# Optimization experiments

Measured on AMD Instinct MI355X. Metric: run time of the kernel, lower is better.

Reference implementation:

```python
import jax, jax.numpy as jnp
import numpy as np

EPS = 1e-5

def _silu(x):
    return x * jax.nn.sigmoid(x)

def _layernorm(x, g, b):
    mu = jnp.mean(x, axis=-1, keepdims=True)
    var = jnp.mean((x - mu) ** 2, axis=-1, keepdims=True)
    return (x - mu) * jax.lax.rsqrt(var + EPS) * g + b

def _mamba(x, in_w, conv_w, conv_b, xproj_w, dt_w, dt_b, A_log, Dp, out_w):
    # x: (B, L, dm); faithful mamba-ssm block: in_proj -> causal dwconv -> silu ->
    # x_proj -> softplus(dt_proj) -> selective scan -> gate -> out_proj
    B, L, dm = x.shape
    di, K = conv_w.shape          # d_inner, d_conv
    ds = A_log.shape[1]           # d_state
    dtr = dt_w.shape[1]           # dt_rank
    xz = x @ in_w.T               # (B, L, 2*di)
    xi, z = jnp.split(xz, 2, axis=-1)
    # causal depthwise conv1d (pad K-1 on the left), kernel unrolled (K=4)
    xpad = jnp.pad(xi, ((0, 0), (K - 1, 0), (0, 0)))
    xc = conv_b + sum(conv_w[:, k] * xpad[:, k:k + L, :] for k in range(K))
    xc = _silu(xc)                # (B, L, di)
    xdbl = xc @ xproj_w.T         # (B, L, dtr + 2*ds)
    dt, Bm, Cm = jnp.split(xdbl, [dtr, dtr + ds], axis=-1)
    delta = jax.nn.softplus(dt @ dt_w.T + dt_b)        # (B, L, di)
    A = -jnp.exp(A_log)                                # (di, ds)
    dA = jnp.exp(delta[..., None] * A)                 # (B, L, di, ds)
    dBu = delta[..., None] * Bm[:, :, None, :] * xc[..., None]
    def step(h, inp):
        dA_t, dBu_t, C_t = inp                         # (B,di,ds),(B,di,ds),(B,ds)
        h = dA_t * h + dBu_t
        y = jnp.einsum('bdn,bn->bd', h, C_t)
        return h, y
    h0 = jnp.zeros((B, di, ds), dtype=x.dtype)
    _, ys = jax.lax.scan(step, h0, (dA.transpose(1, 0, 2, 3),
                                    dBu.transpose(1, 0, 2, 3),
                                    Cm.transpose(1, 0, 2)))
    y = ys.transpose(1, 0, 2) + xc * Dp                # (B, L, di)
    y = y * _silu(z)
    return y @ out_w.T                                 # (B, L, dm)

def _forward(t1, t2, t3, t4, t5,
             m0_in_w, m0_conv_w, m0_conv_b, m0_xproj_w, m0_dt_w, m0_dt_b, m0_Alog, m0_D, m0_out_w,
             m1_in_w, m1_conv_w, m1_conv_b, m1_xproj_w, m1_dt_w, m1_dt_b, m1_Alog, m1_D, m1_out_w,
             norm_g, norm_b, proj_w, proj_b, norm1_g, norm1_b, proj1_w, proj1_b, skip_scale):
    B = t1.shape[0]
    flat = lambda t, c: t.reshape(B, c, -1).transpose(0, 2, 1)   # (B, N, C)
    f1, f2, f3, f4, f5 = flat(t1, 8), flat(t2, 16), flat(t3, 24), flat(t4, 32), flat(t5, 48)
    c1 = jnp.concatenate([f1[:, :, 0:8], f2[:, :, 0:8], f3[:, :, 0:8], f4[:, :, 0:8], f5[:, :, 0:8]], axis=1)   # (B,21824,8)
    c2 = jnp.concatenate([f2[:, :, 8:16], f3[:, :, 8:16], f4[:, :, 8:16], f5[:, :, 8:16]], axis=1)              # (B,5440,8)
    c3 = jnp.concatenate([f3[:, :, 16:24], f4[:, :, 16:24], f5[:, :, 16:24]], axis=1)                           # (B,1344,8)
    c4 = jnp.concatenate([f4[:, :, 24:32], f5[:, :, 24:32]], axis=1)                                            # (B,320,8)
    c5 = f5[:, :, 32:48]                                                                                        # (B,64,16)
    def block8(c):
        y = _mamba(c, m0_in_w, m0_conv_w, m0_conv_b, m0_xproj_w, m0_dt_w, m0_dt_b, m0_Alog, m0_D, m0_out_w)
        return _layernorm(y + skip_scale * c, norm_g, norm_b) @ proj_w.T + proj_b
    x1m, x2m, x3m, x4m = block8(c1), block8(c2), block8(c3), block8(c4)
    y5 = _mamba(c5, m1_in_w, m1_conv_w, m1_conv_b, m1_xproj_w, m1_dt_w, m1_dt_b, m1_Alog, m1_D, m1_out_w)
    x5m = _layernorm(y5 + skip_scale * c5, norm1_g, norm1_b) @ proj1_w.T + proj1_b
    a1 = x1m[:, 0:16384, :]
    a2 = jnp.concatenate([x1m[:, 16384:20480, :], x2m[:, 0:4096, :]], axis=2)
    a3 = jnp.concatenate([x1m[:, 20480:21504, :], x2m[:, 4096:5120, :], x3m[:, 0:1024, :]], axis=2)
    a4 = jnp.concatenate([x1m[:, 21504:21760, :], x2m[:, 5120:5376, :], x3m[:, 1024:1280, :], x4m[:, 0:256, :]], axis=2)
    a5 = jnp.concatenate([x1m[:, 21760:, :], x2m[:, 5376:, :], x3m[:, 1280:, :], x4m[:, 256:, :], x5m], axis=2)
    x1 = a1.transpose(0, 2, 1).reshape(B, 8, 128, 128)
    x2 = a2.transpose(0, 2, 1).reshape(B, 16, 64, 64)
    x3 = a3.transpose(0, 2, 1).reshape(B, 24, 32, 32)
    x4 = a4.transpose(0, 2, 1).reshape(B, 32, 16, 16)
    x5 = a5.transpose(0, 2, 1).reshape(B, 48, 8, 8)
    return (x1, x2, x3, x4, x5)

def setup_inputs() -> dict:
    key = jax.random.key(0)
    ks = iter(jax.random.split(key, 64))
    B = 8
    def n(shape, s=1.0):
        return jax.random.normal(next(ks), shape, dtype=jnp.float32) * s
    inp = {
        't1': n((B, 8, 128, 128)), 't2': n((B, 16, 64, 64)), 't3': n((B, 24, 32, 32)),
        't4': n((B, 32, 16, 16)), 't5': n((B, 48, 8, 8)),
    }
    def mamba_params(pfx, dm):
        di, ds, K, dtr = 2 * dm, 16, 4, 1  # expand=2, d_state=16, d_conv=4, dt_rank=ceil(dm/16)=1
        return {
            pfx + '_in_w': n((2 * di, dm), dm ** -0.5),
            pfx + '_conv_w': n((di, K), 0.3),
            pfx + '_conv_b': n((di,), 0.1),
            pfx + '_xproj_w': n((dtr + 2 * ds, di), di ** -0.5),
            pfx + '_dt_w': n((di, dtr), 1.0),
            pfx + '_dt_b': n((di,), 0.1) - 3.0,
            pfx + '_Alog': jnp.log(jnp.tile(jnp.arange(1.0, ds + 1.0, dtype=jnp.float32), (di, 1))),
            pfx + '_D': jnp.ones((di,), jnp.float32),
            pfx + '_out_w': n((dm, di), di ** -0.5),
        }
    inp.update(mamba_params('m0', 8))
    inp.update(mamba_params('m1', 16))
    inp.update({
        'norm_g': jnp.ones((8,), jnp.float32), 'norm_b': jnp.zeros((8,), jnp.float32),
        'proj_w': n((8, 8), 8 ** -0.5), 'proj_b': jnp.zeros((8,), jnp.float32),
        'norm1_g': jnp.ones((16,), jnp.float32), 'norm1_b': jnp.zeros((16,), jnp.float32),
        'proj1_w': n((16, 16), 16 ** -0.5), 'proj1_b': jnp.zeros((16,), jnp.float32),
        'skip_scale': jnp.ones((1,), jnp.float32),
    })
    return inp

def reference(t1, t2, t3, t4, t5,
              m0_in_w, m0_conv_w, m0_conv_b, m0_xproj_w, m0_dt_w, m0_dt_b, m0_Alog, m0_D, m0_out_w,
              m1_in_w, m1_conv_w, m1_conv_b, m1_xproj_w, m1_dt_w, m1_dt_b, m1_Alog, m1_D, m1_out_w,
              norm_g, norm_b, proj_w, proj_b, norm1_g, norm1_b, proj1_w, proj1_b, skip_scale):
    return _forward(t1, t2, t3, t4, t5,
                    m0_in_w, m0_conv_w, m0_conv_b, m0_xproj_w, m0_dt_w, m0_dt_b, m0_Alog, m0_D, m0_out_w,
                    m1_in_w, m1_conv_w, m1_conv_b, m1_xproj_w, m1_dt_w, m1_dt_b, m1_Alog, m1_D, m1_out_w,
                    norm_g, norm_b, proj_w, proj_b, norm1_g, norm1_b, proj1_w, proj1_b, skip_scale)
```

## Files before the change

kernel.cpp:

```cpp
#include <hip/hip_runtime.h>
#include <cmath>

#define SCH 128
#define SUB 32
#define NCB 228
#define NCHUNK 1824
#define NSUB 7296
#define CPB 2
#define NBLK 912
#define SW_IN 0
#define SW_CONVW 256
#define SW_CONVB 320
#define SW_XPROJ 336
#define SW_DTW 864
#define SW_DTB 880
#define SW_A 896
#define SW_D 1152
#define SW_OUTW 1168
#define SW_NG 1296
#define SW_NB 1304
#define SW_PW 1312
#define SW_PB 1376
#define SW_SKIP 1384
#define REC 1392
#define XP8 5872
#define GRECW 5004
#define YOF 6396
#define SMEM3 8572
#define V_IN 0
#define V_CONVW 1024
#define V_CONVB 1152
#define V_XPROJ 1184
#define V_DTW 2240
#define V_DTB 2272
#define V_A 2304
#define V_D 2816
#define V_OUTW 2848
#define V_NG 3360
#define V_NB 3376
#define V_PW 3392
#define V_PB 3648
#define V_SKIP 3664
#define V_XC 3668
#define V_DL 5780
#define V_BM 7892
#define V_CM 8916
#define SMEMP1 9940

struct Params {
  const float *t0, *t1, *t2, *t3, *t4;
  const float *in_w0,*conv_w0,*conv_b0,*xproj0,*dtw0,*dtb0,*Alog0,*D0,*outw0;
  const float *in_w1,*conv_w1,*conv_b1,*xproj1,*dtw1,*dtb1,*Alog1,*D1,*outw1;
  const float *ng,*nb,*pw,*pb,*n1g,*n1b,*p1w,*p1b,*skip;
  float* out;
  float *hloc, *sumdelta, *grec;
};

__device__ __forceinline__ float softplusf(float x) { return x > 20.f ? x : log1pf(__expf(x)); }
__device__ __forceinline__ float siluf(float x) { return x * (1.f / (1.f + __expf(-x))); }
__device__ __forceinline__ unsigned pk(float a, float b) {
  unsigned ua = __float_as_uint(a) + 0x8000u;
  unsigned ub = __float_as_uint(b) + 0x8000u;
  return (ua >> 16) | (ub & 0xFFFF0000u);
}
__device__ __forceinline__ float lo16(unsigned w) { return __uint_as_float(w << 16); }
__device__ __forceinline__ float hi16(unsigned w) { return __uint_as_float(w & 0xFFFF0000u); }

struct Loc { int k, pos, ch, hw, C; };

__device__ __forceinline__ Loc locate(int seq, int l) {
  Loc r;
  if (seq == 0) { r.ch = 0;
    if (l < 16384)      { r.k=0; r.pos=l;        r.hw=16384; r.C=8;  }
    else if (l < 20480) { r.k=1; r.pos=l-16384;  r.hw=4096;  r.C=16; }
    else if (l < 21504) { r.k=2; r.pos=l-20480;  r.hw=1024;  r.C=24; }
    else if (l < 21760) { r.k=3; r.pos=l-21504;  r.hw=256;   r.C=32; }
    else                { r.k=4; r.pos=l-21760;  r.hw=64;    r.C=48; }
  } else if (seq == 1) { r.ch = 8;
    if (l < 4096)       { r.k=1; r.pos=l;        r.hw=4096;  r.C=16; }
    else if (l < 5120)  { r.k=2; r.pos=l-4096;   r.hw=1024;  r.C=24; }
    else if (l < 5376)  { r.k=3; r.pos=l-5120;   r.hw=256;   r.C=32; }
    else                { r.k=4; r.pos=l-5376;   r.hw=64;    r.C=48; }
  } else if (seq == 2) { r.ch = 16;
    if (l < 1024)       { r.k=2; r.pos=l;        r.hw=1024;  r.C=24; }
    else if (l < 1280)  { r.k=3; r.pos=l-1024;   r.hw=256;   r.C=32; }
    else                { r.k=4; r.pos=l-1280;   r.hw=64;    r.C=48; }
  } else { r.ch = 24;
    if (l < 256)        { r.k=3; r.pos=l;        r.hw=256;   r.C=32; }
    else                { r.k=4; r.pos=l-256;    r.hw=64;    r.C=48; }
  }
  return r;
}

__device__ __forceinline__ const float* tsel(const Params& p, int k) {
  switch (k) { case 0: return p.t0; case 1: return p.t1; case 2: return p.t2;
               case 3: return p.t3; default: return p.t4; }
}
__device__ __forceinline__ int outbase(int k) {
  switch (k) { case 0: return 0; case 1: return 1048576; case 2: return 1572864;
               case 3: return 1769472; default: return 1835008; }
}

__device__ __forceinline__ void gather8(const Params& p, int b, int seq, int l, float* c) {
  Loc lc = locate(seq, l);
  const float* t = tsel(p, lc.k);
  int base = (b * lc.C + lc.ch) * lc.hw + lc.pos;
  #pragma unroll
  for (int j = 0; j < 8; ++j) c[j] = t[base + j * lc.hw];
}

__device__ __forceinline__ void decode_bid(int bid, int& b, int& seq, int& l0, int& Sa) {
  b = bid / NCB;
  int r = bid - b * NCB;
  int c, L;
  if (r < 171)      { seq = 0; c = r;       L = 21824; }
  else if (r < 214) { seq = 1; c = r - 171; L = 5440;  }
  else if (r < 225) { seq = 2; c = r - 214; L = 1344;  }
  else              { seq = 3; c = r - 225; L = 320;   }
  l0 = c * SCH;
  int rem = L - l0;
  Sa = rem < SCH ? rem : SCH;
}

__device__ void load_w0(const Params& p, float* s, int tid) {
  for (int i = tid; i < 256; i += 256) s[SW_IN + i] = p.in_w0[i];
  for (int i = tid; i < 64;  i += 256) s[SW_CONVW + i] = p.conv_w0[i];
  for (int i = tid; i < 16;  i += 256) s[SW_CONVB + i] = p.conv_b0[i];
  for (int i = tid; i < 528; i += 256) s[SW_XPROJ + i] = p.xproj0[i];
  for (int i = tid; i < 16;  i += 256) s[SW_DTW + i] = p.dtw0[i];
  for (int i = tid; i < 16;  i += 256) s[SW_DTB + i] = p.dtb0[i];
  for (int i = tid; i < 256; i += 256) s[SW_A + i] = -__expf(p.Alog0[i]);
  for (int i = tid; i < 16;  i += 256) s[SW_D + i] = p.D0[i];
  for (int i = tid; i < 128; i += 256) s[SW_OUTW + i] = p.outw0[i];
  for (int i = tid; i < 8;   i += 256) s[SW_NG + i] = p.ng[i];
  for (int i = tid; i < 8;   i += 256) s[SW_NB + i] = p.nb[i];
  for (int i = tid; i < 64;  i += 256) s[SW_PW + i] = p.pw[i];
  for (int i = tid; i < 8;   i += 256) s[SW_PB + i] = p.pb[i];
  if (tid == 0) s[SW_SKIP] = p.skip[0];
}

__device__ __forceinline__ float dot16h(const float* w, int ch0, int cho,
                                        const float* a, const float* o) {
  float4 wa0 = *(const float4*)&w[ch0];
  float4 wa1 = *(const float4*)&w[ch0 + 4];
  float4 wb0 = *(const float4*)&w[cho];
  float4 wb1 = *(const float4*)&w[cho + 4];
  float r = wa0.x * a[0];
  r = fmaf(wa0.y, a[1], r); r = fmaf(wa0.z, a[2], r); r = fmaf(wa0.w, a[3], r);
  r = fmaf(wa1.x, a[4], r); r = fmaf(wa1.y, a[5], r);
  r = fmaf(wa1.z, a[6], r); r = fmaf(wa1.w, a[7], r);
  r = fmaf(wb0.x, o[0], r); r = fmaf(wb0.y, o[1], r);
  r = fmaf(wb0.z, o[2], r); r = fmaf(wb0.w, o[3], r);
  r = fmaf(wb1.x, o[4], r); r = fmaf(wb1.y, o[5], r);
  r = fmaf(wb1.z, o[6], r); r = fmaf(wb1.w, o[7], r);
  return r;
}

__device__ void stage1(const Params& p, float* s, int b, int seq, int l0, int Sa, int tid) {
  int tok = tid >> 1, hf = tid & 1;
  int ch0 = hf * 8, cho = 8 - ch0;
  if (tok < Sa + 3) {
    int l = l0 - 3 + tok;
    float x8[8];
    if (l >= 0) gather8(p, b, seq, l, x8);
    else {
      #pragma unroll
      for (int j = 0; j < 8; ++j) x8[j] = 0.f;
    }
    #pragma unroll
    for (int ii = 0; ii < 8; ++ii) {
      int i = ch0 + ii;
      float4 wa = *(const float4*)&s[SW_IN + i * 8];
      float4 wb = *(const float4*)&s[SW_IN + i * 8 + 4];
      float a = wa.x * x8[0];
      a = fmaf(wa.y, x8[1], a); a = fmaf(wa.z, x8[2], a); a = fmaf(wa.w, x8[3], a);
      a = fmaf(wb.x, x8[4], a); a = fmaf(wb.y, x8[5], a);
      a = fmaf(wb.z, x8[6], a); a = fmaf(wb.w, x8[7], a);
      s[REC + tok * 17 + i] = a;
    }
    if (hf == 0) {
      unsigned* xp = (unsigned*)&s[XP8 + tok * 4];
      #pragma unroll
      for (int q = 0; q < 4; ++q) xp[q] = pk(x8[2*q], x8[2*q + 1]);
    }
  }
  if (Sa == SCH && tok >= SCH - 3) {
    int r = tok + 3;
    int l = l0 - 3 + r;
    float x8[8];
    gather8(p, b, seq, l, x8);
    #pragma unroll
    for (int ii = 0; ii < 8; ++ii) {
      int i = ch0 + ii;
      float4 wa = *(const float4*)&s[SW_IN + i * 8];
      float4 wb = *(const float4*)&s[SW_IN + i * 8 + 4];
      float a = wa.x * x8[0];
      a = fmaf(wa.y, x8[1], a); a = fmaf(wa.z, x8[2], a); a = fmaf(wa.w, x8[3], a);
      a = fmaf(wb.x, x8[4], a); a = fmaf(wb.y, x8[5], a);
      a = fmaf(wb.z, x8[6], a); a = fmaf(wb.w, x8[7], a);
      s[REC + r * 17 + i] = a;
    }
    if (hf == 0) {
      unsigned* xp = (unsigned*)&s[XP8 + r * 4];
      #pragma unroll
      for (int q = 0; q < 4; ++q) xp[q] = pk(x8[2*q], x8[2*q + 1]);
    }
  }
  __syncthreads();
  bool act = tok < Sa;
  float xc8[8], xco[8];
  float dt = 0.f;
  if (act) {
    #pragma unroll
    for (int ii = 0; ii < 8; ++ii) {
      int i = ch0 + ii;
      float4 cw = *(const float4*)&s[SW_CONVW + i * 4];
      float a = s[SW_CONVB + i];
      a = fmaf(cw.x, s[REC + (tok + 0) * 17 + i], a);
      a = fmaf(cw.y, s[REC + (tok + 1) * 17 + i], a);
      a = fmaf(cw.z, s[REC + (tok + 2) * 17 + i], a);
      a = fmaf(cw.w, s[REC + (tok + 3) * 17 + i], a);
      xc8[ii] = siluf(a);
    }
    #pragma unroll
    for (int ii = 0; ii < 8; ++ii) xco[ii] = __shfl_xor(xc8[ii], 1);
    dt = dot16h(&s[SW_XPROJ], ch0, cho, xc8, xco);
  }
  __syncthreads();
  unsigned* ru = (unsigned*)&s[REC + tok * 35];
  if (act) {
    #pragma unroll
    for (int q = 0; q < 4; ++q) {
      int d0 = ch0 + 2 * q;
      float da = softplusf(fmaf(dt, s[SW_DTW + d0],     s[SW_DTB + d0]));
      float db = softplusf(fmaf(dt, s[SW_DTW + d0 + 1], s[SW_DTB + d0 + 1]));
      ru[hf * 4 + q]     = pk(da, db);
      ru[8 + hf * 4 + q] = pk(xc8[2*q], xc8[2*q + 1]);
    }
    #pragma unroll
    for (int q = 0; q < 4; ++q) {
      int n0 = ch0 + 2 * q;
      float a0 = dot16h(&s[SW_XPROJ + (1 + n0) * 16], ch0, cho, xc8, xco);
      float a1 = dot16h(&s[SW_XPROJ + (2 + n0) * 16], ch0, cho, xc8, xco);
      ru[16 + hf * 4 + q] = pk(a0, a1);
    }
    #pragma unroll
    for (int q = 0; q < 4; ++q) {
      int n0 = ch0 + 2 * q;
      float a0 = dot16h(&s[SW_XPROJ + (17 + n0) * 16], ch0, cho, xc8, xco);
      float a1 = dot16h(&s[SW_XPROJ + (18 + n0) * 16], ch0, cho, xc8, xco);
      ru[24 + hf * 4 + q] = pk(a0, a1);
    }
  } else {
    #pragma unroll
    for (int q = 0; q < 4; ++q) {
      ru[hf * 4 + q] = 0u;
      ru[8 + hf * 4 + q] = 0u;
      ru[16 + hf * 4 + q] = 0u;
      ru[24 + hf * 4 + q] = 0u;
    }
  }
  __syncthreads();
}

__device__ void load_w1(const Params& p, float* s, int tid) {
  for (int i = tid; i < 1024; i += 256) s[V_IN + i] = p.in_w1[i];
  for (int i = tid; i < 128;  i += 256) s[V_CONVW + i] = p.conv_w1[i];
  for (int i = tid; i < 32;   i += 256) s[V_CONVB + i] = p.conv_b1[i];
  for (int i = tid; i < 1056; i += 256) s[V_XPROJ + i] = p.xproj1[i];
  for (int i = tid; i < 32;   i += 256) s[V_DTW + i] = p.dtw1[i];
  for (int i = tid; i < 32;   i += 256) s[V_DTB + i] = p.dtb1[i];
  for (int i = tid; i < 512;  i += 256) s[V_A + i] = -__expf(p.Alog1[i]);
  for (int i = tid; i < 32;   i += 256) s[V_D + i] = p.D1[i];
  for (int i = tid; i < 512;  i += 256) s[V_OUTW + i] = p.outw1[i];
  for (int i = tid; i < 16;   i += 256) s[V_NG + i] = p.n1g[i];
  for (int i = tid; i < 16;   i += 256) s[V_NB + i] = p.n1b[i];
  for (int i = tid; i < 256;  i += 256) s[V_PW + i] = p.p1w[i];
  for (int i = tid; i < 16;   i += 256) s[V_PB + i] = p.p1b[i];
  if (tid == 0) s[V_SKIP] = p.skip[0];
}

__device__ void c5_path(const Params& p, float* s, int b, int tid) {
  load_w1(p, s, tid);
  int og = tid >> 6, tok = tid & 63;
  float x16[16];
  #pragma unroll
  for (int j = 0; j < 16; ++j) x16[j] = p.t4[(b * 48 + 32 + j) * 64 + tok];
  __syncthreads();
  #pragma unroll
  for (int ii = 0; ii < 8; ++ii) {
    int i = og * 8 + ii;
    float a = 0.f;
    #pragma unroll
    for (int j = 0; j < 16; ++j) a = fmaf(s[V_IN + i * 16 + j], x16[j], a);
    float xm1 = __shfl_up(a, 1);
    float xm2 = __shfl_up(a, 2);
    float xm3 = __shfl_up(a, 3);
    float c = s[V_CONVB + i];
    c = fmaf(s[V_CONVW + i * 4 + 3], a, c);
    if (tok >= 1) c = fmaf(s[V_CONVW + i * 4 + 2], xm1, c);
    if (tok >= 2) c = fmaf(s[V_CONVW + i * 4 + 1], xm2, c);
    if (tok >= 3) c = fmaf(s[V_CONVW + i * 4 + 0], xm3, c);
    s[V_XC + tok * 33 + i] = siluf(c);
  }
  __syncthreads();
  float xcr[32];
  #pragma unroll
  for (int i = 0; i < 32; ++i) xcr[i] = s[V_XC + tok * 33 + i];
  float dt = 0.f;
  #pragma unroll
  for (int i = 0; i < 32; ++i) dt = fmaf(s[V_XPROJ + i], xcr[i], dt);
  #pragma unroll
  for (int nn = 0; nn < 4; ++nn) {
    int n = og * 4 + nn;
    float aB = 0.f, aC = 0.f;
    #pragma unroll
    for (int i = 0; i < 32; ++i) {
      aB = fmaf(s[V_XPROJ + (1 + n) * 32 + i], xcr[i], aB);
      aC = fmaf(s[V_XPROJ + (17 + n) * 32 + i], xcr[i], aC);
    }
    s[V_BM + tok * 16 + n] = aB;
    s[V_CM + tok * 16 + n] = aC;
  }
  #pragma unroll
  for (int ii = 0; ii < 8; ++ii) {
    int d = og * 8 + ii;
    s[V_DL + tok * 33 + d] = softplusf(fmaf(dt, s[V_DTW + d], s[V_DTB + d]));
  }
  __syncthreads();
  if (tid < 128) {
    int d = tid >> 2, ng = tid & 3;
    float4 Av = *(float4*)&s[V_A + d * 16 + ng * 4];
    float h0 = 0.f, h1 = 0.f, h2 = 0.f, h3 = 0.f;
    for (int tile = 0; tile < 16; ++tile) {
      int tb = tile * 4;
      float dl[4], xv[4]; float4 bm[4], cm[4];
      #pragma unroll
      for (int i = 0; i < 4; ++i) {
        dl[i] = s[V_DL + (tb + i) * 33 + d];
        xv[i] = s[V_XC + (tb + i) * 33 + d];
        bm[i] = *(float4*)&s[V_BM + (tb + i) * 16 + ng * 4];
        cm[i] = *(float4*)&s[V_CM + (tb + i) * 16 + ng * 4];
      }
      float yp[4];
      #pragma unroll
      for (int i = 0; i < 4; ++i) {
        float u = dl[i] * xv[i];
        float e0 = __expf(Av.x * dl[i]), e1 = __expf(Av.y * dl[i]);
        float e2 = __expf(Av.z * dl[i]), e3 = __expf(Av.w * dl[i]);
        h0 = fmaf(e0, h0, u * bm[i].x);
        h1 = fmaf(e1, h1, u * bm[i].y);
        h2 = fmaf(e2, h2, u * bm[i].z);
        h3 = fmaf(e3, h3, u * bm[i].w);
        float y = h0 * cm[i].x;
        y = fmaf(h1, cm[i].y, y); y = fmaf(h2, cm[i].z, y); y = fmaf(h3, cm[i].w, y);
        yp[i] = y;
      }
      #pragma unroll
      for (int i = 0; i < 4; ++i) yp[i] += __shfl_xor(yp[i], 1);
      #pragma unroll
      for (int i = 0; i < 4; ++i) yp[i] += __shfl_xor(yp[i], 2);
      float ysel = ng == 0 ? yp[0] : ng == 1 ? yp[1] : ng == 2 ? yp[2] : yp[3];
      s[V_DL + (tb + ng) * 33 + d] = ysel;
    }
  }
  __syncthreads();
  #pragma unroll
  for (int ii = 0; ii < 8; ++ii) {
    int d = og * 8 + ii;
    float z = 0.f;
    #pragma unroll
    for (int j = 0; j < 16; ++j) z = fmaf(s[V_IN + (32 + d) * 16 + j], x16[j], z);
    float yv = (s[V_DL + tok * 33 + d] + s[V_XC + tok * 33 + d] * s[V_D + d]) * siluf(z);
    s[V_DL + tok * 33 + d] = yv;
  }
  __syncthreads();
  float yr[32];
  #pragma unroll
  for (int d = 0; d < 32; ++d) yr[d] = s[V_DL + tok * 33 + d];
  float sk = s[V_SKIP];
  #pragma unroll
  for (int mm = 0; mm < 4; ++mm) {
    int m = og * 4 + mm;
    float a = sk * x16[m];
    #pragma unroll
    for (int d = 0; d < 32; ++d) a = fmaf(s[V_OUTW + m * 32 + d], yr[d], a);
    s[V_XC + tok * 33 + m] = a;
  }
  __syncthreads();
  if (tid < 64) {
    float ov[16];
    #pragma unroll
    for (int m = 0; m < 16; ++m) ov[m] = s[V_XC + tok * 33 + m];
    float mu = 0.f;
    #pragma unroll
    for (int m = 0; m < 16; ++m) mu += ov[m];
    mu *= (1.f / 16.f);
    float var = 0.f;
    #pragma unroll
    for (int m = 0; m < 16; ++m) { float t = ov[m] - mu; var += t * t; }
    var *= (1.f / 16.f);
    float inv = rsqrtf(var + 1e-5f);
    #pragma unroll
    for (int m = 0; m < 16; ++m)
      s[V_XC + tok * 33 + m] = (ov[m] - mu) * inv * s[V_NG + m] + s[V_NB + m];
  }
  __syncthreads();
  float lr[16];
  #pragma unroll
  for (int j = 0; j < 16; ++j) lr[j] = s[V_XC + tok * 33 + j];
  #pragma unroll
  for (int mm = 0; mm < 4; ++mm) {
    int m = og * 4 + mm;
    float a = s[V_PB + m];
    #pragma unroll
    for (int j = 0; j < 16; ++j) a = fmaf(s[V_PW + m * 16 + j], lr[j], a);
    p.out[1835008 + (b * 48 + 32 + m) * 64 + tok] = a;
  }
}

__global__ __launch_bounds__(256, 3) void k_pass1(Params p) {
  __shared__ float s[SMEMP1];
  int tid = threadIdx.x;
  if (blockIdx.x < 8) { c5_path(p, s, blockIdx.x, tid); return; }
  load_w0(p, s, tid);
  int w = tid >> 6, lane = tid & 63;
  int d = lane >> 2, ng = lane & 3;
  int dh = d >> 1;
  bool dodd = d & 1;
  int t0 = w * SUB;
  const unsigned* su = (const unsigned*)s;
  for (int it = 0; it < CPB; ++it) {
    int cid = (blockIdx.x - 8) * CPB + it;
    int b, seq, l0, Sa;
    decode_bid(cid, b, seq, l0, Sa);
    __syncthreads();
    stage1(p, s, b, seq, l0, Sa, tid);
    {
      uint4* g4 = (uint4*)(p.grec + (size_t)cid * GRECW);
      const uint4* s4 = (const uint4*)&su[REC];
      #pragma unroll 2
      for (int i4 = tid; i4 < GRECW / 4; i4 += 256) g4[i4] = s4[i4];
    }
    float4 Av = *(float4*)&s[SW_A + d * 16 + ng * 4];
    float h0 = 0.f, h1 = 0.f, h2 = 0.f, h3 = 0.f, sd = 0.f;
    for (int tile = 0; tile < 8; ++tile) {
      int tb = t0 + tile * 4;
      unsigned wd[4], wx[4]; uint2 wB[4];
      #pragma unroll
      for (int i = 0; i < 4; ++i) {
        int base = REC + (tb + i) * 35;
        wd[i] = su[base + dh];
        wx[i] = su[base + 8 + dh];
        wB[i] = *(const uint2*)&su[base + 16 + ng * 2];
      }
      #pragma unroll
      for (int i = 0; i < 4; ++i) {
        float dl = dodd ? hi16(wd[i]) : lo16(wd[i]);
        float u = dl * (dodd ? hi16(wx[i]) : lo16(wx[i]));
        float e0 = __expf(Av.x * dl), e1 = __expf(Av.y * dl);
        float e2 = __expf(Av.z * dl), e3 = __expf(Av.w * dl);
        h0 = fmaf(e0, h0, u * lo16(wB[i].x));
        h1 = fmaf(e1, h1, u * hi16(wB[i].x));
        h2 = fmaf(e2, h2, u * lo16(wB[i].y));
        h3 = fmaf(e3, h3, u * hi16(wB[i].y));
        sd += dl;
      }
    }
    int gs = cid * 4 + w;
    unsigned* hu = (unsigned*)p.hloc;
    hu[gs * 128 + d * 8 + ng * 2]     = pk(h0, h1);
    hu[gs * 128 + d * 8 + ng * 2 + 1] = pk(h2, h3);
    if (ng == 0) p.sumdelta[(size_t)gs * 16 + d] = sd;
  }
}

__global__ __launch_bounds__(256) void k_pass2(Params p) {
  __shared__ unsigned sh[684 * 8];
  __shared__ float ssd[684];
  __shared__ float sS[32];
  __shared__ float sH[512];
  int bid = blockIdx.x, tid = threadIdx.x;
  int b = bid >> 6;
  int r = bid & 63;
  int seq = r >> 4, d = r & 15;
  const int nch[4] = {171, 43, 11, 3};
  const int chf[4] = {0, 171, 214, 225};
  int nsub = nch[seq] * 4;
  int g0 = (b * NCB + chf[seq]) * 4;
  unsigned* hu = (unsigned*)p.hloc;
  int n8 = nsub * 8;
  for (int wdx = tid; wdx < n8; wdx += 256) {
    int rec = wdx >> 3, pr_ = wdx & 7;
    sh[wdx] = hu[(size_t)(g0 + rec) * 128 + d * 8 + pr_];
  }
  for (int rec = tid; rec < nsub; rec += 256)
    ssd[rec] = p.sumdelta[(size_t)(g0 + rec) * 16 + d];
  int g = tid >> 3, pr = tid & 7;
  float A0 = -__expf(p.Alog0[d * 16 + pr * 2]);
  float A1 = -__expf(p.Alog0[d * 16 + pr * 2 + 1]);
  __syncthreads();
  int T = (nsub + 31) >> 5;
  int i0 = g * T;
  int i1 = i0 + T; if (i1 > nsub) i1 = nsub;
  float S = 0.f, h0 = 0.f, h1 = 0.f;
  for (int i = i0; i < i1; ++i) {
    unsigned wl = sh[i * 8 + pr];
    float sv = ssd[i];
    float e0 = __expf(A0 * sv), e1 = __expf(A1 * sv);
    h0 = fmaf(e0, h0, lo16(wl));
    h1 = fmaf(e1, h1, hi16(wl));
    S += sv;
  }
  if (pr == 0) sS[g] = S;
  sH[g * 16 + pr * 2]     = h0;
  sH[g * 16 + pr * 2 + 1] = h1;
  __syncthreads();
  float q0 = 0.f, q1 = 0.f;
  for (int j = 0; j < g; ++j) {
    float Sj = sS[j];
    float e0 = __expf(A0 * Sj), e1 = __expf(A1 * Sj);
    q0 = fmaf(e0, q0, sH[j * 16 + pr * 2]);
    q1 = fmaf(e1, q1, sH[j * 16 + pr * 2 + 1]);
  }
  for (int i = i0; i < i1; ++i) {
    unsigned wl = sh[i * 8 + pr];
    float sv = ssd[i];
    sh[i * 8 + pr] = pk(q0, q1);
    float e0 = __expf(A0 * sv), e1 = __expf(A1 * sv);
    q0 = fmaf(e0, q0, lo16(wl));
    q1 = fmaf(e1, q1, hi16(wl));
  }
  __syncthreads();
  for (int wdx = tid; wdx < n8; wdx += 256) {
    int rec = wdx >> 3, pr_ = wdx & 7;
    hu[(size_t)(g0 + rec) * 128 + d * 8 + pr_] = sh[wdx];
  }
}

__global__ __launch_bounds__(256, 3) void k_pass3(Params p) {
  __shared__ float s[SMEM3];
  int tid = threadIdx.x;
  load_w0(p, s, tid);
  int w = tid >> 6, lane = tid & 63;
  int d = lane >> 2, ng = lane & 3;
  int dh = d >> 1;
  bool dodd = d & 1;
  int t0 = w * SUB;
  int tok = tid >> 1, hf = tid & 1, ch0 = hf * 8;
  const unsigned* su = (const unsigned*)s;
  for (int it = 0; it < CPB; ++it) {
    int cid = blockIdx.x * CPB + it;
    int b, seq, l0, Sa;
    decode_bid(cid, b, seq, l0, Sa);
    __syncthreads();
    {
      const uint4* g4 = (const uint4*)(p.grec + (size_t)cid * GRECW);
      uint4* s4 = (uint4*)&((unsigned*)s)[REC];
      #pragma unroll 2
      for (int i4 = tid; i4 < GRECW / 4; i4 += 256) s4[i4] = g4[i4];
    }
    __syncthreads();
    int gs = cid * 4 + w;
    float4 Av = *(float4*)&s[SW_A + d * 16 + ng * 4];
    const unsigned* hu = (const unsigned*)p.hloc;
    unsigned hw0 = hu[gs * 128 + d * 8 + ng * 2];
    unsigned hw1 = hu[gs * 128 + d * 8 + ng * 2 + 1];
    float h0 = lo16(hw0), h1 = hi16(hw0), h2 = lo16(hw1), h3 = hi16(hw1);
    for (int tile = 0; tile < 8; ++tile) {
      int tb = t0 + tile * 4;
      unsigned wd[4], wx[4]; uint2 wB[4], wC[4];
      #pragma unroll
      for (int i = 0; i < 4; ++i) {
        int base = REC + (tb + i) * 35;
        wd[i] = su[base + dh];
        wx[i] = su[base + 8 + dh];
        wB[i] = *(const uint2*)&su[base + 16 + ng * 2];
        wC[i] = *(const uint2*)&su[base + 24 + ng * 2];
      }
      float yp[4];
      #pragma unroll
      for (int i = 0; i < 4; ++i) {
        float dl = dodd ? hi16(wd[i]) : lo16(wd[i]);
        float u = dl * (dodd ? hi16(wx[i]) : lo16(wx[i]));
        float e0 = __expf(Av.x * dl), e1 = __expf(Av.y * dl);
        float e2 = __expf(Av.z * dl), e3 = __expf(Av.w * dl);
        h0 = fmaf(e0, h0, u * lo16(wB[i].x));
        h1 = fmaf(e1, h1, u * hi16(wB[i].x));
        h2 = fmaf(e2, h2, u * lo16(wB[i].y));
        h3 = fmaf(e3, h3, u * hi16(wB[i].y));
        float y = h0 * lo16(wC[i].x);
        y = fmaf(h1, hi16(wC[i].x), y);
        y = fmaf(h2, lo16(wC[i].y), y);
        y = fmaf(h3, hi16(wC[i].y), y);
        yp[i] = y;
      }
      #pragma unroll
      for (int i = 0; i < 4; ++i) yp[i] += __shfl_xor(yp[i], 1);
      #pragma unroll
      for (int i = 0; i < 4; ++i) yp[i] += __shfl_xor(yp[i], 2);
      float ysel = ng == 0 ? yp[0] : ng == 1 ? yp[1] : ng == 2 ? yp[2] : yp[3];
      s[YOF + (tb + ng) * 17 + d] = ysel;
    }
    __syncthreads();
    if (tok < Sa) {
      const unsigned* xp = (const unsigned*)&s[XP8 + (tok + 3) * 4];
      float c8[8];
      #pragma unroll
      for (int q = 0; q < 4; ++q) { c8[2*q] = lo16(xp[q]); c8[2*q+1] = hi16(xp[q]); }
      const unsigned* ru = (const unsigned*)&s[REC + tok * 35];
      float yv8[8];
      #pragma unroll
      for (int q = 0; q < 4; ++q) {
        unsigned wv = ru[8 + hf * 4 + q];
        int d0 = ch0 + 2 * q;
        float4 w0a = *(const float4*)&s[SW_IN + (16 + d0) * 8];
        float4 w0b = *(const float4*)&s[SW_IN + (16 + d0) * 8 + 4];
        float4 w1a = *(const float4*)&s[SW_IN + (17 + d0) * 8];
        float4 w1b = *(const float4*)&s[SW_IN + (17 + d0) * 8 + 4];
        float z0 = w0a.x * c8[0];
        z0 = fmaf(w0a.y, c8[1], z0); z0 = fmaf(w0a.z, c8[2], z0); z0 = fmaf(w0a.w, c8[3], z0);
        z0 = fmaf(w0b.x, c8[4], z0); z0 = fmaf(w0b.y, c8[5], z0);
        z0 = fmaf(w0b.z, c8[6], z0); z0 = fmaf(w0b.w, c8[7], z0);
        float z1 = w1a.x * c8[0];
        z1 = fmaf(w1a.y, c8[1], z1); z1 = fmaf(w1a.z, c8[2], z1); z1 = fmaf(w1a.w, c8[3], z1);
        z1 = fmaf(w1b.x, c8[4], z1); z1 = fmaf(w1b.y, c8[5], z1);
        z1 = fmaf(w1b.z, c8[6], z1); z1 = fmaf(w1b.w, c8[7], z1);
        yv8[2*q]   = (s[YOF + tok * 17 + d0]     + lo16(wv) * s[SW_D + d0])     * siluf(z0);
        yv8[2*q+1] = (s[YOF + tok * 17 + d0 + 1] + hi16(wv) * s[SW_D + d0 + 1]) * siluf(z1);
      }
      float o[8];
      float sk = s[SW_SKIP];
      #pragma unroll
      for (int m = 0; m < 8; ++m) {
        float4 wv0 = *(const float4*)&s[SW_OUTW + m * 16 + ch0];
        float4 wv1 = *(const float4*)&s[SW_OUTW + m * 16 + ch0 + 4];
        float a = wv0.x * yv8[0];
        a = fmaf(wv0.y, yv8[1], a); a = fmaf(wv0.z, yv8[2], a); a = fmaf(wv0.w, yv8[3], a);
        a = fmaf(wv1.x, yv8[4], a); a = fmaf(wv1.y, yv8[5], a);
        a = fmaf(wv1.z, yv8[6], a); a = fmaf(wv1.w, yv8[7], a);
        a += __shfl_xor(a, 1);
        o[m] = a + sk * c8[m];
      }
      float mu = 0.f;
      #pragma unroll
      for (int m = 0; m < 8; ++m) mu += o[m];
      mu *= 0.125f;
      float var = 0.f;
      #pragma unroll
      for (int m = 0; m < 8; ++m) { float t = o[m] - mu; var += t * t; }
      var *= 0.125f;
      float inv = rsqrtf(var + 1e-5f);
      #pragma unroll
      for (int m = 0; m < 8; ++m) o[m] = (o[m] - mu) * inv * s[SW_NG + m] + s[SW_NB + m];
      Loc lc = locate(seq, l0 + tok);
      int obase = outbase(lc.k) + (b * lc.C + lc.ch) * lc.hw + lc.pos;
      #pragma unroll
      for (int mm = 0; mm < 4; ++mm) {
        int m = hf * 4 + mm;
        float4 pw0 = *(const float4*)&s[SW_PW + m * 8];
        float4 pw1 = *(const float4*)&s[SW_PW + m * 8 + 4];
        float a = s[SW_PB + m];
        a = fmaf(pw0.x, o[0], a); a = fmaf(pw0.y, o[1], a);
        a = fmaf(pw0.z, o[2], a); a = fmaf(pw0.w, o[3], a);
        a = fmaf(pw1.x, o[4], a); a = fmaf(pw1.y, o[5], a);
        a = fmaf(pw1.z, o[6], a); a = fmaf(pw1.w, o[7], a);
        p.out[obase + m * lc.hw] = a;
      }
    }
  }
}

extern "C" void kernel_launch(void* const* d_in, const int* in_sizes, int n_in,
                              void* d_out, int out_size, void* d_ws, size_t ws_size,
                              hipStream_t stream) {
  (void)in_sizes; (void)n_in; (void)out_size; (void)ws_size;
  Params p;
  p.t0 = (const float*)d_in[0];  p.t1 = (const float*)d_in[1];
  p.t2 = (const float*)d_in[2];  p.t3 = (const float*)d_in[3];
  p.t4 = (const float*)d_in[4];
  p.in_w0   = (const float*)d_in[5];
  p.conv_w0 = (const float*)d_in[6];
  p.conv_b0 = (const float*)d_in[7];
  p.xproj0  = (const float*)d_in[8];
  p.dtw0    = (const float*)d_in[9];
  p.dtb0    = (const float*)d_in[10];
  p.Alog0   = (const float*)d_in[11];
  p.D0      = (const float*)d_in[12];
  p.outw0   = (const float*)d_in[13];
  p.in_w1   = (const float*)d_in[14];
  p.conv_w1 = (const float*)d_in[15];
  p.conv_b1 = (const float*)d_in[16];
  p.xproj1  = (const float*)d_in[17];
  p.dtw1    = (const float*)d_in[18];
  p.dtb1    = (const float*)d_in[19];
  p.Alog1   = (const float*)d_in[20];
  p.D1      = (const float*)d_in[21];
  p.outw1   = (const float*)d_in[22];
  p.ng  = (const float*)d_in[23];
  p.nb  = (const float*)d_in[24];
  p.pw  = (const float*)d_in[25];
  p.pb  = (const float*)d_in[26];
  p.n1g = (const float*)d_in[27];
  p.n1b = (const float*)d_in[28];
  p.p1w = (const float*)d_in[29];
  p.p1b = (const float*)d_in[30];
  p.skip = (const float*)d_in[31];
  p.out = (float*)d_out;
  float* ws = (float*)d_ws;
  p.hloc     = ws;
  p.sumdelta = ws + (size_t)NSUB * 128;
  p.grec     = ws + (size_t)NSUB * 128 + (size_t)NSUB * 16;
  k_pass1<<<dim3(NBLK + 8), dim3(256), 0, stream>>>(p);
  k_pass2<<<dim3(512), dim3(256), 0, stream>>>(p);
  k_pass3<<<dim3(NBLK), dim3(256), 0, stream>>>(p);
}
```

Baseline: 130.6 us.

## Rebalance scan passes: one chunk per pass1 block, move c5 path to pass2, use exp2

Pass1 now runs one chunk per block over 1824 blocks with a smaller shared-memory footprint and a launch bound targeting higher occupancy. The separate c5 mamba path moves from pass1 into pass2, where it runs alongside the inter-chunk prefix scan. A is pre-scaled by log2(e) so every exp becomes a native exp2, saving one multiply per exponential. Pass3's launch bound is raised to 4 blocks per SM, which may force register spills.

```diff
diff --git a/kernel.cpp b/kernel.cpp
--- a/kernel.cpp
+++ b/kernel.cpp
@@ -6,8 +6,10 @@
 #define NCB 228
 #define NCHUNK 1824
 #define NSUB 7296
-#define CPB 2
-#define NBLK 912
+#define CPB3 2
+#define NBLK3 912
+#define LOG2E 1.442695041f
+#define EXP2F(x) __builtin_exp2f(x)
 #define SW_IN 0
 #define SW_CONVW 256
 #define SW_CONVB 320
@@ -26,6 +28,7 @@
 #define XP8 5872
 #define GRECW 5004
 #define YOF 6396
+#define SMEMP1 6396
 #define SMEM3 8572
 #define V_IN 0
 #define V_CONVW 1024
@@ -45,7 +48,7 @@
 #define V_DL 5780
 #define V_BM 7892
 #define V_CM 8916
-#define SMEMP1 9940
+#define SMEMP2 9940
 
 struct Params {
   const float *t0, *t1, *t2, *t3, *t4;
@@ -129,7 +132,7 @@
   for (int i = tid; i < 528; i += 256) s[SW_XPROJ + i] = p.xproj0[i];
   for (int i = tid; i < 16;  i += 256) s[SW_DTW + i] = p.dtw0[i];
   for (int i = tid; i < 16;  i += 256) s[SW_DTB + i] = p.dtb0[i];
-  for (int i = tid; i < 256; i += 256) s[SW_A + i] = -__expf(p.Alog0[i]);
+  for (int i = tid; i < 256; i += 256) s[SW_A + i] = -__expf(p.Alog0[i]) * LOG2E;
   for (int i = tid; i < 16;  i += 256) s[SW_D + i] = p.D0[i];
   for (int i = tid; i < 128; i += 256) s[SW_OUTW + i] = p.outw0[i];
   for (int i = tid; i < 8;   i += 256) s[SW_NG + i] = p.ng[i];
@@ -263,6 +266,59 @@
   __syncthreads();
 }
 
+__global__ __launch_bounds__(256, 6) void k_pass1(Params p) {
+  __shared__ float s[SMEMP1];
+  int tid = threadIdx.x;
+  load_w0(p, s, tid);
+  int w = tid >> 6, lane = tid & 63;
+  int d = lane >> 2, ng = lane & 3;
+  int dh = d >> 1;
+  bool dodd = d & 1;
+  int t0 = w * SUB;
+  const unsigned* su = (const unsigned*)s;
+  int cid = blockIdx.x;
+  int b, seq, l0, Sa;
+  decode_bid(cid, b, seq, l0, Sa);
+  __syncthreads();
+  stage1(p, s, b, seq, l0, Sa, tid);
+  {
+    uint4* g4 = (uint4*)(p.grec + (size_t)cid * GRECW);
+    const uint4* s4 = (const uint4*)&su[REC];
+    #pragma unroll 2
+    for (int i4 = tid; i4 < GRECW / 4; i4 += 256) g4[i4] = s4[i4];
+  }
+  float4 Av = *(float4*)&s[SW_A + d * 16 + ng * 4];
+  float h0 = 0.f, h1 = 0.f, h2 = 0.f, h3 = 0.f, sd = 0.f;
+  for (int tile = 0; tile < 8; ++tile) {
+    int tb = t0 + tile * 4;
+    unsigned wd[4], wx[4]; uint2 wB[4];
+    #pragma unroll
+    for (int i = 0; i < 4; ++i) {
+      int base = REC + (tb + i) * 35;
+      wd[i] = su[base + dh];
+      wx[i] = su[base + 8 + dh];
+      wB[i] = *(const uint2*)&su[base + 16 + ng * 2];
+    }
+    #pragma unroll
+    for (int i = 0; i < 4; ++i) {
+      float dl = dodd ? hi16(wd[i]) : lo16(wd[i]);
+      float u = dl * (dodd ? hi16(wx[i]) : lo16(wx[i]));
+      float e0 = EXP2F(Av.x * dl), e1 = EXP2F(Av.y * dl);
+      float e2 = EXP2F(Av.z * dl), e3 = EXP2F(Av.w * dl);
+      h0 = fmaf(e0, h0, u * lo16(wB[i].x));
+      h1 = fmaf(e1, h1, u * hi16(wB[i].x));
+      h2 = fmaf(e2, h2, u * lo16(wB[i].y));
+      h3 = fmaf(e3, h3, u * hi16(wB[i].y));
+      sd += dl;
+    }
+  }
+  int gs = cid * 4 + w;
+  unsigned* hu = (unsigned*)p.hloc;
+  hu[gs * 128 + d * 8 + ng * 2]     = pk(h0, h1);
+  hu[gs * 128 + d * 8 + ng * 2 + 1] = pk(h2, h3);
+  if (ng == 0) p.sumdelta[(size_t)gs * 16 + d] = sd;
+}
+
 __device__ void load_w1(const Params& p, float* s, int tid) {
   for (int i = tid; i < 1024; i += 256) s[V_IN + i] = p.in_w1[i];
   for (int i = tid; i < 128;  i += 256) s[V_CONVW + i] = p.conv_w1[i];
@@ -270,7 +326,7 @@
   for (int i = tid; i < 1056; i += 256) s[V_XPROJ + i] = p.xproj1[i];
   for (int i = tid; i < 32;   i += 256) s[V_DTW + i] = p.dtw1[i];
   for (int i = tid; i < 32;   i += 256) s[V_DTB + i] = p.dtb1[i];
-  for (int i = tid; i < 512;  i += 256) s[V_A + i] = -__expf(p.Alog1[i]);
+  for (int i = tid; i < 512;  i += 256) s[V_A + i] = -__expf(p.Alog1[i]) * LOG2E;
   for (int i = tid; i < 32;   i += 256) s[V_D + i] = p.D1[i];
   for (int i = tid; i < 512;  i += 256) s[V_OUTW + i] = p.outw1[i];
   for (int i = tid; i < 16;   i += 256) s[V_NG + i] = p.n1g[i];
@@ -346,8 +402,8 @@
       #pragma unroll
       for (int i = 0; i < 4; ++i) {
         float u = dl[i] * xv[i];
-        float e0 = __expf(Av.x * dl[i]), e1 = __expf(Av.y * dl[i]);
-        float e2 = __expf(Av.z * dl[i]), e3 = __expf(Av.w * dl[i]);
+        float e0 = EXP2F(Av.x * dl[i]), e1 = EXP2F(Av.y * dl[i]);
+        float e2 = EXP2F(Av.z * dl[i]), e3 = EXP2F(Av.w * dl[i]);
         h0 = fmaf(e0, h0, u * bm[i].x);
         h1 = fmaf(e1, h1, u * bm[i].y);
         h2 = fmaf(e2, h2, u * bm[i].z);
@@ -419,71 +475,18 @@
   }
 }
 
-__global__ __launch_bounds__(256, 3) void k_pass1(Params p) {
-  __shared__ float s[SMEMP1];
-  int tid = threadIdx.x;
-  if (blockIdx.x < 8) { c5_path(p, s, blockIdx.x, tid); return; }
-  load_w0(p, s, tid);
-  int w = tid >> 6, lane = tid & 63;
-  int d = lane >> 2, ng = lane & 3;
-  int dh = d >> 1;
-  bool dodd = d & 1;
-  int t0 = w * SUB;
-  const unsigned* su = (const unsigned*)s;
-  for (int it = 0; it < CPB; ++it) {
-    int cid = (blockIdx.x - 8) * CPB + it;
-    int b, seq, l0, Sa;
-    decode_bid(cid, b, seq, l0, Sa);
-    __syncthreads();
-    stage1(p, s, b, seq, l0, Sa, tid);
-    {
-      uint4* g4 = (uint4*)(p.grec + (size_t)cid * GRECW);
-      const uint4* s4 = (const uint4*)&su[REC];
-      #pragma unroll 2
-      for (int i4 = tid; i4 < GRECW / 4; i4 += 256) g4[i4] = s4[i4];
-    }
-    float4 Av = *(float4*)&s[SW_A + d * 16 + ng * 4];
-    float h0 = 0.f, h1 = 0.f, h2 = 0.f, h3 = 0.f, sd = 0.f;
-    for (int tile = 0; tile < 8; ++tile) {
-      int tb = t0 + tile * 4;
-      unsigned wd[4], wx[4]; uint2 wB[4];
-      #pragma unroll
-      for (int i = 0; i < 4; ++i) {
-        int base = REC + (tb + i) * 35;
-        wd[i] = su[base + dh];
-        wx[i] = su[base + 8 + dh];
-        wB[i] = *(const uint2*)&su[base + 16 + ng * 2];
-      }
-      #pragma unroll
-      for (int i = 0; i < 4; ++i) {
-        float dl = dodd ? hi16(wd[i]) : lo16(wd[i]);
-        float u = dl * (dodd ? hi16(wx[i]) : lo16(wx[i]));
-        float e0 = __expf(Av.x * dl), e1 = __expf(Av.y * dl);
-        float e2 = __expf(Av.z * dl), e3 = __expf(Av.w * dl);
-        h0 = fmaf(e0, h0, u * lo16(wB[i].x));
-        h1 = fmaf(e1, h1, u * hi16(wB[i].x));
-        h2 = fmaf(e2, h2, u * lo16(wB[i].y));
-        h3 = fmaf(e3, h3, u * hi16(wB[i].y));
-        sd += dl;
-      }
-    }
-    int gs = cid * 4 + w;
-    unsigned* hu = (unsigned*)p.hloc;
-    hu[gs * 128 + d * 8 + ng * 2]     = pk(h0, h1);
-    hu[gs * 128 + d * 8 + ng * 2 + 1] = pk(h2, h3);
-    if (ng == 0) p.sumdelta[(size_t)gs * 16 + d] = sd;
-  }
-}
-
 __global__ __launch_bounds__(256) void k_pass2(Params p) {
-  __shared__ unsigned sh[684 * 8];
-  __shared__ float ssd[684];
-  __shared__ float sS[32];
-  __shared__ float sH[512];
+  __shared__ float s[SMEMP2];
   int bid = blockIdx.x, tid = threadIdx.x;
-  int b = bid >> 6;
-  int r = bid & 63;
-  int seq = r >> 4, d = r & 15;
+  if (bid < 8) { c5_path(p, s, bid, tid); return; }
+  unsigned* sh = (unsigned*)&s[0];
+  float* ssd = &s[5472];
+  float* sS = &s[6156];
+  float* sH = &s[6188];
+  int r = bid - 8;
+  int b = r >> 6;
+  int rr = r & 63;
+  int seq = rr >> 4, d = rr & 15;
   const int nch[4] = {171, 43, 11, 3};
   const int chf[4] = {0, 171, 214, 225};
   int nsub = nch[seq] * 4;
@@ -497,8 +500,8 @@
   for (int rec = tid; rec < nsub; rec += 256)
     ssd[rec] = p.sumdelta[(size_t)(g0 + rec) * 16 + d];
   int g = tid >> 3, pr = tid & 7;
-  float A0 = -__expf(p.Alog0[d * 16 + pr * 2]);
-  float A1 = -__expf(p.Alog0[d * 16 + pr * 2 + 1]);
+  float A0 = -__expf(p.Alog0[d * 16 + pr * 2]) * LOG2E;
+  float A1 = -__expf(p.Alog0[d * 16 + pr * 2 + 1]) * LOG2E;
   __syncthreads();
   int T = (nsub + 31) >> 5;
   int i0 = g * T;
@@ -507,7 +510,7 @@
   for (int i = i0; i < i1; ++i) {
     unsigned wl = sh[i * 8 + pr];
     float sv = ssd[i];
-    float e0 = __expf(A0 * sv), e1 = __expf(A1 * sv);
+    float e0 = EXP2F(A0 * sv), e1 = EXP2F(A1 * sv);
     h0 = fmaf(e0, h0, lo16(wl));
     h1 = fmaf(e1, h1, hi16(wl));
     S += sv;
@@ -519,7 +522,7 @@
   float q0 = 0.f, q1 = 0.f;
   for (int j = 0; j < g; ++j) {
     float Sj = sS[j];
-    float e0 = __expf(A0 * Sj), e1 = __expf(A1 * Sj);
+    float e0 = EXP2F(A0 * Sj), e1 = EXP2F(A1 * Sj);
     q0 = fmaf(e0, q0, sH[j * 16 + pr * 2]);
     q1 = fmaf(e1, q1, sH[j * 16 + pr * 2 + 1]);
   }
@@ -527,7 +530,7 @@
     unsigned wl = sh[i * 8 + pr];
     float sv = ssd[i];
     sh[i * 8 + pr] = pk(q0, q1);
-    float e0 = __expf(A0 * sv), e1 = __expf(A1 * sv);
+    float e0 = EXP2F(A0 * sv), e1 = EXP2F(A1 * sv);
     q0 = fmaf(e0, q0, lo16(wl));
     q1 = fmaf(e1, q1, hi16(wl));
   }
@@ -538,7 +541,7 @@
   }
 }
 
-__global__ __launch_bounds__(256, 3) void k_pass3(Params p) {
+__global__ __launch_bounds__(256, 4) void k_pass3(Params p) {
   __shared__ float s[SMEM3];
   int tid = threadIdx.x;
   load_w0(p, s, tid);
@@ -549,8 +552,8 @@
   int t0 = w * SUB;
   int tok = tid >> 1, hf = tid & 1, ch0 = hf * 8;
   const unsigned* su = (const unsigned*)s;
-  for (int it = 0; it < CPB; ++it) {
-    int cid = blockIdx.x * CPB + it;
+  for (int it = 0; it < CPB3; ++it) {
+    int cid = blockIdx.x * CPB3 + it;
     int b, seq, l0, Sa;
     decode_bid(cid, b, seq, l0, Sa);
     __syncthreads();
@@ -583,8 +586,8 @@
       for (int i = 0; i < 4; ++i) {
         float dl = dodd ? hi16(wd[i]) : lo16(wd[i]);
         float u = dl * (dodd ? hi16(wx[i]) : lo16(wx[i]));
-        float e0 = __expf(Av.x * dl), e1 = __expf(Av.y * dl);
-        float e2 = __expf(Av.z * dl), e3 = __expf(Av.w * dl);
+        float e0 = EXP2F(Av.x * dl), e1 = EXP2F(Av.y * dl);
+        float e2 = EXP2F(Av.z * dl), e3 = EXP2F(Av.w * dl);
         h0 = fmaf(e0, h0, u * lo16(wB[i].x));
         h1 = fmaf(e1, h1, u * hi16(wB[i].x));
         h2 = fmaf(e2, h2, u * lo16(wB[i].y));
@@ -711,7 +714,7 @@
   p.hloc     = ws;
   p.sumdelta = ws + (size_t)NSUB * 128;
   p.grec     = ws + (size_t)NSUB * 128 + (size_t)NSUB * 16;
-  k_pass1<<<dim3(NBLK + 8), dim3(256), 0, stream>>>(p);
-  k_pass2<<<dim3(512), dim3(256), 0, stream>>>(p);
-  k_pass3<<<dim3(NBLK), dim3(256), 0, stream>>>(p);
-}
+  k_pass1<<<dim3(NCHUNK), dim3(256), 0, stream>>>(p);
+  k_pass2<<<dim3(8 + 512), dim3(256), 0, stream>>>(p);
+  k_pass3<<<dim3(NBLK3), dim3(256), 0, stream>>>(p);
+}
```

New measurement: 141.8 us. 8.6% more time.
